# Kernel optimization log

Hardware: AMD Instinct MI355X
Metric: run time of the kernel (lower is better)

Reference implementation:

```python
import jax, jax.numpy as jnp
import numpy as np

EPS = 1e-6
D_CONV = 4

def _layernorm(x):
    m = jnp.mean(x, axis=-1, keepdims=True)
    v = jnp.mean((x - m) ** 2, axis=-1, keepdims=True)
    return (x - m) / jnp.sqrt(v + EPS)

def setup_inputs() -> dict:
    key = jax.random.key(0)
    ks = jax.random.split(key, 20)
    B, L, D = 2, 4096, 1024
    Di = D          # expand = 1
    N = 16          # d_state
    R = 64          # dt_rank = ceil(D/16)
    H = 4 * D       # mlp hidden
    s = 0.02
    rn = lambda k, sh: s * jax.random.normal(k, sh, dtype=jnp.float32)
    x = jax.random.normal(ks[0], (B, L, D), dtype=jnp.float32)
    path = jax.random.permutation(ks[1], L).astype(jnp.int32)
    path_rev = jnp.argsort(path).astype(jnp.int32)
    A_log = jnp.log(jnp.tile(jnp.arange(1, N + 1, dtype=jnp.float32)[None, :], (Di, 1)))
    return {
        'x': x, 'path': path, 'path_rev': path_rev,
        'in_proj_w': rn(ks[2], (2 * Di, D)),
        'conv_w': rn(ks[3], (Di, D_CONV)), 'conv_b': rn(ks[4], (Di,)),
        'x_proj_w': rn(ks[5], (R + 2 * N, Di)),
        'dt_proj_w': rn(ks[6], (Di, R)), 'dt_proj_b': rn(ks[7], (Di,)),
        'A_log': A_log, 'D_param': jnp.ones((Di,), dtype=jnp.float32),
        'out_proj_w': rn(ks[8], (D, Di)),
        'fc1_w': rn(ks[9], (H, D)), 'fc1_b': jnp.zeros((H,), dtype=jnp.float32),
        'fc2_w': rn(ks[10], (D, H)), 'fc2_b': jnp.zeros((D,), dtype=jnp.float32),
    }

def _mamba(u, in_proj_w, conv_w, conv_b, x_proj_w, dt_proj_w, dt_proj_b, A_log, D_param, out_proj_w):
    B, L, _ = u.shape
    N = A_log.shape[1]
    R = dt_proj_w.shape[1]
    xz = u @ in_proj_w.T                      # (B,L,2*Di)
    xi, z = jnp.split(xz, 2, axis=-1)
    # causal depthwise conv1d, kernel 4
    xpad = jnp.pad(xi, ((0, 0), (D_CONV - 1, 0), (0, 0)))
    xc = conv_b + sum(conv_w[:, k] * xpad[:, k:k + L, :] for k in range(D_CONV))
    xc = jax.nn.silu(xc)                      # (B,L,Di)
    proj = xc @ x_proj_w.T                    # (B,L,R+2N)
    dt_r = proj[..., :R]
    Bm = proj[..., R:R + N]                   # (B,L,N)
    Cm = proj[..., R + N:]                    # (B,L,N)
    dt = jax.nn.softplus(dt_r @ dt_proj_w.T + dt_proj_b)  # (B,L,Di)
    A = -jnp.exp(A_log)                       # (Di,N)

    def step(h, inp):
        dt_t, B_t, C_t, x_t = inp             # (B,Di),(B,N),(B,N),(B,Di)
        dA = jnp.exp(dt_t[:, :, None] * A)    # (B,Di,N)
        h = dA * h + (dt_t * x_t)[:, :, None] * B_t[:, None, :]
        y = jnp.einsum('bdn,bn->bd', h, C_t)
        return h, y

    h0 = jnp.zeros((B, xc.shape[-1], N), dtype=u.dtype)
    xs = (dt.transpose(1, 0, 2), Bm.transpose(1, 0, 2), Cm.transpose(1, 0, 2), xc.transpose(1, 0, 2))
    _, ys = jax.lax.scan(step, h0, xs)        # (L,B,Di)
    y = ys.transpose(1, 0, 2) + D_param * xc
    y = y * jax.nn.silu(z)
    return y @ out_proj_w.T

def reference(x, path, path_rev, in_proj_w, conv_w, conv_b, x_proj_w, dt_proj_w, dt_proj_b,
              A_log, D_param, out_proj_w, fc1_w, fc1_b, fc2_w, fc2_b):
    tmp1 = x[:, path, :]                      # zigzag gather
    tmp1 = _mamba(_layernorm(tmp1), in_proj_w, conv_w, conv_b, x_proj_w,
                  dt_proj_w, dt_proj_b, A_log, D_param, out_proj_w)
    x = x + tmp1[:, path_rev, :]              # zigzag scatter (inverse gather)
    h = _layernorm(x)
    h = jax.nn.gelu(h @ fc1_w.T + fc1_b, approximate=True) @ fc2_w.T + fc2_b
    return x + h
```

## Files before the change

### kernel.cpp

```cpp
#include <hip/hip_runtime.h>
#include <cstdint>
#include <cstddef>

typedef unsigned short u16;
typedef __bf16 bf16x8 __attribute__((ext_vector_type(8)));
typedef float f32x4 __attribute__((ext_vector_type(4)));

#define B_ 2
#define L_ 4096
#define D_ 1024
#define N_ 16
#define BL_ 8192
#define NC_ 64
#define LC_ 64

__device__ __forceinline__ float bf2f(u16 h) {
  union { unsigned int u; float f; } v; v.u = ((unsigned int)h) << 16; return v.f;
}
__device__ __forceinline__ u16 f2bf(float f) {
  union { float f; unsigned int u; } v; v.f = f;
  unsigned int r = v.u + 0x7FFFu + ((v.u >> 16) & 1u);
  return (u16)(r >> 16);
}
__device__ __forceinline__ float sigmoidf_(float x) { return 1.0f / (1.0f + __expf(-x)); }

#define WBF_TOT 11730944
__global__ __launch_bounds__(256) void cvt_w_k(
    const float* __restrict__ s0, const float* __restrict__ s1,
    const float* __restrict__ s2, const float* __restrict__ s3,
    const float* __restrict__ s4, const float* __restrict__ s5,
    u16* __restrict__ dst)
{
  int i = blockIdx.x * 256 + threadIdx.x;
  if (i >= WBF_TOT) return;
  float v;
  if (i < 2097152) v = s0[i];
  else if (i < 2228224) { int j = i - 2097152; v = (j < 98304) ? s1[j] : 0.0f; }
  else if (i < 2293760) v = s2[i - 2228224];
  else if (i < 3342336) v = s3[i - 2293760];
  else if (i < 7536640) v = s4[i - 3342336];
  else v = s5[i - 7536640];
  dst[i] = f2bf(v);
}

#define BM 128
#define BN 128
#define BK 32

enum { M_BF16 = 0, M_PROJ = 1, M_SOFTPLUS = 2, M_GELU = 3, M_BIASRES = 4 };

#define GLDS(gp, lp) __builtin_amdgcn_global_load_lds( \
    (const __attribute__((address_space(1))) void*)(gp), \
    (__attribute__((address_space(3))) void*)(lp), 16, 0, 0)

template<int MODE>
__global__ __launch_bounds__(256) void gemm_bt(
    const u16* __restrict__ A, const u16* __restrict__ W,
    float* __restrict__ C, u16* __restrict__ C2,
    const float* __restrict__ bias, const float* __restrict__ resid,
    int M, int N, int K)
{
  __shared__ __align__(16) u16 As[2][BM * BK];
  __shared__ __align__(16) u16 Bs[2][BN * BK];

  const int id = blockIdx.x + gridDim.x * blockIdx.y;
  const int xcd = id & 7;
  const int q = id >> 3;
  const int bandH = gridDim.y >> 3;
  const int xs = q % gridDim.x;
  const int ys = xcd * bandH + q / gridDim.x;
  const int bm = ys * BM;
  const int bn = xs * BN;

  const int tid = threadIdx.x;
  const int lane = tid & 63;
  const int wave = tid >> 6;
  const int wr = (wave >> 1) * 64;
  const int wc = (wave & 1) * 64;

  f32x4 acc[4][4];
#pragma unroll
  for (int i = 0; i < 4; ++i)
#pragma unroll
    for (int j = 0; j < 4; ++j)
#pragma unroll
      for (int r = 0; r < 4; ++r) acc[i][j][r] = 0.0f;

  const int r0 = tid >> 2;
  const int ke = (tid & 3) << 3;
  const u16* Ab = A + (size_t)(bm + r0) * K + ke;
  const u16* Wb = W + (size_t)(bn + r0) * K + ke;
  const size_t rstep = (size_t)64 * K;

  auto issue = [&](int buf, int k0) {
    GLDS(Ab + k0, &As[buf][tid * 8]);
    GLDS(Ab + k0 + rstep, &As[buf][(tid + 256) * 8]);
    GLDS(Wb + k0, &Bs[buf][tid * 8]);
    GLDS(Wb + k0 + rstep, &Bs[buf][(tid + 256) * 8]);
  };

  issue(0, 0);
  int cur = 0;
  const int kq = (lane >> 4) << 3;
  const int mr = lane & 15;
  for (int k0 = 0; k0 < K; k0 += BK) {
    __syncthreads();
    if (k0 + BK < K) issue(cur ^ 1, k0 + BK);
    bf16x8 af[4], bfr[4];
#pragma unroll
    for (int i = 0; i < 4; ++i)
      af[i] = *(const bf16x8*)(&As[cur][(wr + i * 16 + mr) * BK + kq]);
#pragma unroll
    for (int j = 0; j < 4; ++j)
      bfr[j] = *(const bf16x8*)(&Bs[cur][(wc + j * 16 + mr) * BK + kq]);
#pragma unroll
    for (int i = 0; i < 4; ++i)
#pragma unroll
      for (int j = 0; j < 4; ++j)
        acc[i][j] = __builtin_amdgcn_mfma_f32_16x16x32_bf16(af[i], bfr[j], acc[i][j], 0, 0, 0);
    cur ^= 1;
  }

  const int mlo = (lane >> 4) << 2;
  const int nlo = lane & 15;
#pragma unroll
  for (int i = 0; i < 4; ++i) {
#pragma unroll
    for (int j = 0; j < 4; ++j) {
      int col = bn + wc + j * 16 + nlo;
      if (col < N) {
#pragma unroll
        for (int r = 0; r < 4; ++r) {
          int row = bm + wr + i * 16 + mlo + r;
          float v = acc[i][j][r];
          if constexpr (MODE == M_BF16) {
            C2[(size_t)row * N + col] = f2bf(v);
          } else if constexpr (MODE == M_PROJ) {
            C[(size_t)row * 96 + col] = v;
            if (col < 64) C2[((size_t)row << 6) + col] = f2bf(v);
          } else if constexpr (MODE == M_SOFTPLUS) {
            v += bias[col];
            C[(size_t)row * N + col] = (v > 20.0f) ? v : log1pf(__expf(v));
          } else if constexpr (MODE == M_GELU) {
            v += bias[col];
            float a = 0.7978845608028654f * (v + 0.044715f * v * v * v);
            float t = 1.0f - 2.0f / (__expf(2.0f * a) + 1.0f);
            C2[(size_t)row * N + col] = f2bf(0.5f * v * (1.0f + t));
          } else if constexpr (MODE == M_BIASRES) {
            C[(size_t)row * N + col] = v + bias[col] + resid[(size_t)row * N + col];
          }
        }
      }
    }
  }
}

__device__ __forceinline__ void blockReduce2(float& s, float& q) {
#pragma unroll
  for (int o = 32; o > 0; o >>= 1) { s += __shfl_down(s, o, 64); q += __shfl_down(q, o, 64); }
  __shared__ float red[2][4];
  int lane = threadIdx.x & 63, wave = threadIdx.x >> 6;
  if (lane == 0) { red[0][wave] = s; red[1][wave] = q; }
  __syncthreads();
  s = red[0][0] + red[0][1] + red[0][2] + red[0][3];
  q = red[1][0] + red[1][1] + red[1][2] + red[1][3];
}

__global__ __launch_bounds__(256) void ln_gather_k(
    const float* __restrict__ x, const int* __restrict__ path, u16* __restrict__ out)
{
  int b = blockIdx.x >> 12;
  int l = blockIdx.x & 4095;
  int src = path[l];
  const float* row = x + (((size_t)b * L_ + src) << 10);
  u16* orow = out + (((size_t)b * L_ + l) << 10);
  float v[4], s = 0.f, q = 0.f;
#pragma unroll
  for (int i = 0; i < 4; ++i) {
    v[i] = row[threadIdx.x + (i << 8)];
    s += v[i]; q += v[i] * v[i];
  }
  blockReduce2(s, q);
  float mean = s * (1.0f / 1024.0f);
  float var = q * (1.0f / 1024.0f) - mean * mean;
  float rstd = rsqrtf(var + 1e-6f);
#pragma unroll
  for (int i = 0; i < 4; ++i)
    orow[threadIdx.x + (i << 8)] = f2bf((v[i] - mean) * rstd);
}

__global__ __launch_bounds__(256) void ln_scatter_k(
    const float* __restrict__ x, const int* __restrict__ prev,
    const u16* __restrict__ mo, float* __restrict__ xnew, u16* __restrict__ lnout)
{
  int b = blockIdx.x >> 12;
  int l = blockIdx.x & 4095;
  int pl = prev[l];
  const float* xr = x + (((size_t)b * L_ + l) << 10);
  const u16* mr_ = mo + (((size_t)b * L_ + pl) << 10);
  size_t base = ((size_t)blockIdx.x) << 10;
  float v[4], s = 0.f, q = 0.f;
#pragma unroll
  for (int i = 0; i < 4; ++i) {
    v[i] = xr[threadIdx.x + (i << 8)] + bf2f(mr_[threadIdx.x + (i << 8)]);
    s += v[i]; q += v[i] * v[i];
  }
  blockReduce2(s, q);
  float mean = s * (1.0f / 1024.0f);
  float var = q * (1.0f / 1024.0f) - mean * mean;
  float rstd = rsqrtf(var + 1e-6f);
#pragma unroll
  for (int i = 0; i < 4; ++i) {
    xnew[base + threadIdx.x + (i << 8)] = v[i];
    lnout[base + threadIdx.x + (i << 8)] = f2bf((v[i] - mean) * rstd);
  }
}

__global__ __launch_bounds__(256) void conv_silu_k(
    const u16* __restrict__ xz, const float* __restrict__ cw, const float* __restrict__ cb,
    u16* __restrict__ xc)
{
  int idx = blockIdx.x * 256 + threadIdx.x;
  int d = idx & 1023;
  int l = (idx >> 10) & 4095;
  int b = idx >> 22;
  float acc = cb[d];
#pragma unroll
  for (int k = 0; k < 4; ++k) {
    int ls = l + k - 3;
    if (ls >= 0)
      acc += cw[(d << 2) + k] * bf2f(xz[(((size_t)b * L_ + ls) << 11) + d]);
  }
  acc = acc * sigmoidf_(acc);
  xc[idx] = f2bf(acc);
}

__global__ __launch_bounds__(256) void scan_p1_k(
    const float* __restrict__ dt, const u16* __restrict__ xc, const float* __restrict__ proj,
    const float* __restrict__ A_log, float* __restrict__ acum, float* __restrict__ hloc)
{
  int c = blockIdx.x & (NC_ - 1);
  int q = (blockIdx.x >> 6) & 3;
  int b = blockIdx.x >> 8;
  int d = (q << 8) + threadIdx.x;
  float Arow[N_];
#pragma unroll
  for (int n = 0; n < N_; ++n) Arow[n] = -__expf(A_log[(d << 4) + n]);
  float h[N_], ac[N_];
#pragma unroll
  for (int n = 0; n < N_; ++n) { h[n] = 0.0f; ac[n] = 1.0f; }
  int l0 = c << 6;
  for (int i = 0; i < LC_; ++i) {
    size_t rowb = (size_t)b * L_ + (l0 + i);
    float dtv = dt[(rowb << 10) + d];
    float xv = bf2f(xc[(rowb << 10) + d]);
    float dtx = dtv * xv;
    const float* Bp = proj + rowb * 96 + 64;
#pragma unroll
    for (int n = 0; n < N_; ++n) {
      float dA = __expf(dtv * Arow[n]);
      h[n] = dA * h[n] + dtx * Bp[n];
      ac[n] *= dA;
    }
  }
  size_t sb = ((((size_t)b << 10) + d) << 10) + (c << 4);
#pragma unroll
  for (int n = 0; n < N_; ++n) { acum[sb + n] = ac[n]; hloc[sb + n] = h[n]; }
}

__global__ __launch_bounds__(256) void scan_p2_k(
    const float* __restrict__ acum, const float* __restrict__ hloc, float* __restrict__ hin)
{
  int idx = blockIdx.x * 256 + threadIdx.x;
  int n = idx & 15;
  int dn = idx >> 4;
  size_t base = ((size_t)dn << 10) + n;
  float hs = 0.0f;
  for (int c = 0; c < NC_; ++c) {
    hin[base + (c << 4)] = hs;
    hs = acum[base + (c << 4)] * hs + hloc[base + (c << 4)];
  }
}

__global__ __launch_bounds__(256) void scan_p3_k(
    const float* __restrict__ dt, const u16* __restrict__ xc, const float* __restrict__ proj,
    const float* __restrict__ A_log, const float* __restrict__ Dp, const float* __restrict__ hin,
    const u16* __restrict__ xz, u16* __restrict__ yg)
{
  int c = blockIdx.x & (NC_ - 1);
  int q = (blockIdx.x >> 6) & 3;
  int b = blockIdx.x >> 8;
  int d = (q << 8) + threadIdx.x;
  float Arow[N_];
#pragma unroll
  for (int n = 0; n < N_; ++n) Arow[n] = -__expf(A_log[(d << 4) + n]);
  float h[N_];
  size_t sb = ((((size_t)b << 10) + d) << 10) + (c << 4);
#pragma unroll
  for (int n = 0; n < N_; ++n) h[n] = hin[sb + n];
  float Dv = Dp[d];
  int l0 = c << 6;
  for (int i = 0; i < LC_; ++i) {
    size_t rowb = (size_t)b * L_ + (l0 + i);
    float dtv = dt[(rowb << 10) + d];
    float xv = bf2f(xc[(rowb << 10) + d]);
    float dtx = dtv * xv;
    const float* Bp = proj + rowb * 96 + 64;
    const float* Cp = proj + rowb * 96 + 80;
    float y = 0.0f;
#pragma unroll
    for (int n = 0; n < N_; ++n) {
      float dA = __expf(dtv * Arow[n]);
      h[n] = dA * h[n] + dtx * Bp[n];
      y += h[n] * Cp[n];
    }
    y += Dv * xv;
    float zv = bf2f(xz[(rowb << 11) + 1024 + d]);
    yg[(rowb << 10) + d] = f2bf(y * zv * sigmoidf_(zv));
  }
}

extern "C" void kernel_launch(void* const* d_in, const int* in_sizes, int n_in,
                              void* d_out, int out_size, void* d_ws, size_t ws_size,
                              hipStream_t stream)
{
  const float* x_in      = (const float*)d_in[0];
  const int*   path      = (const int*)d_in[1];
  const int*   path_rev  = (const int*)d_in[2];
  const float* in_proj_w = (const float*)d_in[3];
  const float* conv_w    = (const float*)d_in[4];
  const float* conv_b    = (const float*)d_in[5];
  const float* x_proj_w  = (const float*)d_in[6];
  const float* dt_proj_w = (const float*)d_in[7];
  const float* dt_proj_b = (const float*)d_in[8];
  const float* A_log     = (const float*)d_in[9];
  const float* Dp        = (const float*)d_in[10];
  const float* out_pw    = (const float*)d_in[11];
  const float* fc1_w     = (const float*)d_in[12];
  const float* fc1_b     = (const float*)d_in[13];
  const float* fc2_w     = (const float*)d_in[14];
  const float* fc2_b     = (const float*)d_in[15];
  float* out = (float*)d_out;

  char* w = (char*)d_ws;
  size_t off = 0;
  auto alloc = [&](size_t bytes) -> char* {
    char* p = w + off;
    off = (off + bytes + 255) & ~(size_t)255;
    return p;
  };
  u16*   wbf   = (u16*)  alloc((size_t)WBF_TOT * 2);
  u16*   ln_bf = (u16*)  alloc((size_t)BL_ * 1024 * 2);
  u16*   xz    = (u16*)  alloc((size_t)BL_ * 2048 * 2);
  u16*   xc    = (u16*)  alloc((size_t)BL_ * 1024 * 2);
  char*  pool0 = alloc(0);
  float* proj  = (float*)alloc((size_t)BL_ * 96 * 4);
  u16*   dtr   = (u16*)  alloc((size_t)BL_ * 64 * 2);
  float* dt    = (float*)alloc((size_t)BL_ * 1024 * 4);
  float* acum  = (float*)alloc((size_t)2 * 1024 * NC_ * 16 * 4);
  float* hloc  = (float*)alloc((size_t)2 * 1024 * NC_ * 16 * 4);
  float* hin   = (float*)alloc((size_t)2 * 1024 * NC_ * 16 * 4);
  u16*   yg    = (u16*)  alloc((size_t)BL_ * 1024 * 2);
  float* xnew  = (float*)alloc((size_t)BL_ * 1024 * 4);
  u16*   mo    = xz;
  u16*   h1b   = (u16*)pool0;

  const u16* w_inp = wbf;
  const u16* w_xp  = wbf + 2097152;
  const u16* w_dtp = wbf + 2228224;
  const u16* w_op  = wbf + 2293760;
  const u16* w_fc1 = wbf + 3342336;
  const u16* w_fc2 = wbf + 7536640;

  dim3 blk(256);
  cvt_w_k<<<WBF_TOT / 256, blk, 0, stream>>>(in_proj_w, x_proj_w, dt_proj_w, out_pw,
                                             fc1_w, fc2_w, wbf);
  ln_gather_k<<<BL_, blk, 0, stream>>>(x_in, path, ln_bf);
  gemm_bt<M_BF16><<<dim3(16, 64), blk, 0, stream>>>(ln_bf, w_inp, nullptr, xz, nullptr, nullptr, 8192, 2048, 1024);
  conv_silu_k<<<(BL_ * 1024) / 256, blk, 0, stream>>>(xz, conv_w, conv_b, xc);
  gemm_bt<M_PROJ><<<dim3(1, 64), blk, 0, stream>>>(xc, w_xp, proj, dtr, nullptr, nullptr, 8192, 96, 1024);
  gemm_bt<M_SOFTPLUS><<<dim3(8, 64), blk, 0, stream>>>(dtr, w_dtp, dt, nullptr, dt_proj_b, nullptr, 8192, 1024, 64);
  scan_p1_k<<<2 * 4 * NC_, blk, 0, stream>>>(dt, xc, proj, A_log, acum, hloc);
  scan_p2_k<<<(2 * 1024 * 16) / 256, blk, 0, stream>>>(acum, hloc, hin);
  scan_p3_k<<<2 * 4 * NC_, blk, 0, stream>>>(dt, xc, proj, A_log, Dp, hin, xz, yg);
  gemm_bt<M_BF16><<<dim3(8, 64), blk, 0, stream>>>(yg, w_op, nullptr, mo, nullptr, nullptr, 8192, 1024, 1024);
  ln_scatter_k<<<BL_, blk, 0, stream>>>(x_in, path_rev, mo, xnew, ln_bf);
  gemm_bt<M_GELU><<<dim3(32, 64), blk, 0, stream>>>(ln_bf, w_fc1, nullptr, h1b, fc1_b, nullptr, 8192, 4096, 1024);
  gemm_bt<M_BIASRES><<<dim3(8, 64), blk, 0, stream>>>(h1b, w_fc2, out, nullptr, fc2_b, xnew, 8192, 1024, 4096);
}
```

Measured before the change: 638.2 us.

## Triple-buffer GEMM LDS pipeline and store dt and residual in bf16

The GEMM K-loop moves from double to triple buffering. Loads are issued two stages ahead, and __syncthreads is replaced with an explicit vmcnt wait plus s_barrier, so global-to-LDS loads overlap more with MFMA work. Separately, the softplus dt output and the xnew residual are stored as bf16 instead of fp32, which halves their memory traffic in the scan kernels and the fc2 epilogue. The trade-off is lower precision in dt and the residual, more LDS per block (possibly lower occupancy), and a workspace layout where xnew now sits after the h1b region.

```diff
diff --git a/kernel.cpp b/kernel.cpp
--- a/kernel.cpp
+++ b/kernel.cpp
@@ -57,11 +57,11 @@
 __global__ __launch_bounds__(256) void gemm_bt(
     const u16* __restrict__ A, const u16* __restrict__ W,
     float* __restrict__ C, u16* __restrict__ C2,
-    const float* __restrict__ bias, const float* __restrict__ resid,
+    const float* __restrict__ bias, const u16* __restrict__ resid,
     int M, int N, int K)
 {
-  __shared__ __align__(16) u16 As[2][BM * BK];
-  __shared__ __align__(16) u16 Bs[2][BN * BK];
+  __shared__ __align__(16) u16 As[3][BM * BK];
+  __shared__ __align__(16) u16 Bs[3][BN * BK];
 
   const int id = blockIdx.x + gridDim.x * blockIdx.y;
   const int xcd = id & 7;
@@ -100,12 +100,16 @@
   };
 
   issue(0, 0);
+  if (BK < K) issue(1, BK);
   int cur = 0;
   const int kq = (lane >> 4) << 3;
   const int mr = lane & 15;
   for (int k0 = 0; k0 < K; k0 += BK) {
-    __syncthreads();
-    if (k0 + BK < K) issue(cur ^ 1, k0 + BK);
+    if (k0 + BK < K) asm volatile("s_waitcnt vmcnt(4)" ::: "memory");
+    else             asm volatile("s_waitcnt vmcnt(0)" ::: "memory");
+    asm volatile("s_barrier" ::: "memory");
+    int nb = cur + 2; if (nb >= 3) nb -= 3;
+    if (k0 + 2 * BK < K) issue(nb, k0 + 2 * BK);
     bf16x8 af[4], bfr[4];
 #pragma unroll
     for (int i = 0; i < 4; ++i)
@@ -118,7 +122,7 @@
 #pragma unroll
       for (int j = 0; j < 4; ++j)
         acc[i][j] = __builtin_amdgcn_mfma_f32_16x16x32_bf16(af[i], bfr[j], acc[i][j], 0, 0, 0);
-    cur ^= 1;
+    ++cur; if (cur == 3) cur = 0;
   }
 
   const int mlo = (lane >> 4) << 2;
@@ -140,14 +144,15 @@
             if (col < 64) C2[((size_t)row << 6) + col] = f2bf(v);
           } else if constexpr (MODE == M_SOFTPLUS) {
             v += bias[col];
-            C[(size_t)row * N + col] = (v > 20.0f) ? v : log1pf(__expf(v));
+            v = (v > 20.0f) ? v : log1pf(__expf(v));
+            C2[(size_t)row * N + col] = f2bf(v);
           } else if constexpr (MODE == M_GELU) {
             v += bias[col];
             float a = 0.7978845608028654f * (v + 0.044715f * v * v * v);
             float t = 1.0f - 2.0f / (__expf(2.0f * a) + 1.0f);
             C2[(size_t)row * N + col] = f2bf(0.5f * v * (1.0f + t));
           } else if constexpr (MODE == M_BIASRES) {
-            C[(size_t)row * N + col] = v + bias[col] + resid[(size_t)row * N + col];
+            C[(size_t)row * N + col] = v + bias[col] + bf2f(resid[(size_t)row * N + col]);
           }
         }
       }
@@ -191,7 +196,7 @@
 
 __global__ __launch_bounds__(256) void ln_scatter_k(
     const float* __restrict__ x, const int* __restrict__ prev,
-    const u16* __restrict__ mo, float* __restrict__ xnew, u16* __restrict__ lnout)
+    const u16* __restrict__ mo, u16* __restrict__ xnew, u16* __restrict__ lnout)
 {
   int b = blockIdx.x >> 12;
   int l = blockIdx.x & 4095;
@@ -211,7 +216,7 @@
   float rstd = rsqrtf(var + 1e-6f);
 #pragma unroll
   for (int i = 0; i < 4; ++i) {
-    xnew[base + threadIdx.x + (i << 8)] = v[i];
+    xnew[base + threadIdx.x + (i << 8)] = f2bf(v[i]);
     lnout[base + threadIdx.x + (i << 8)] = f2bf((v[i] - mean) * rstd);
   }
 }
@@ -236,7 +241,7 @@
 }
 
 __global__ __launch_bounds__(256) void scan_p1_k(
-    const float* __restrict__ dt, const u16* __restrict__ xc, const float* __restrict__ proj,
+    const u16* __restrict__ dt, const u16* __restrict__ xc, const float* __restrict__ proj,
     const float* __restrict__ A_log, float* __restrict__ acum, float* __restrict__ hloc)
 {
   int c = blockIdx.x & (NC_ - 1);
@@ -252,7 +257,7 @@
   int l0 = c << 6;
   for (int i = 0; i < LC_; ++i) {
     size_t rowb = (size_t)b * L_ + (l0 + i);
-    float dtv = dt[(rowb << 10) + d];
+    float dtv = bf2f(dt[(rowb << 10) + d]);
     float xv = bf2f(xc[(rowb << 10) + d]);
     float dtx = dtv * xv;
     const float* Bp = proj + rowb * 96 + 64;
@@ -283,7 +288,7 @@
 }
 
 __global__ __launch_bounds__(256) void scan_p3_k(
-    const float* __restrict__ dt, const u16* __restrict__ xc, const float* __restrict__ proj,
+    const u16* __restrict__ dt, const u16* __restrict__ xc, const float* __restrict__ proj,
     const float* __restrict__ A_log, const float* __restrict__ Dp, const float* __restrict__ hin,
     const u16* __restrict__ xz, u16* __restrict__ yg)
 {
@@ -302,7 +307,7 @@
   int l0 = c << 6;
   for (int i = 0; i < LC_; ++i) {
     size_t rowb = (size_t)b * L_ + (l0 + i);
-    float dtv = dt[(rowb << 10) + d];
+    float dtv = bf2f(dt[(rowb << 10) + d]);
     float xv = bf2f(xc[(rowb << 10) + d]);
     float dtx = dtv * xv;
     const float* Bp = proj + rowb * 96 + 64;
@@ -356,14 +361,15 @@
   char*  pool0 = alloc(0);
   float* proj  = (float*)alloc((size_t)BL_ * 96 * 4);
   u16*   dtr   = (u16*)  alloc((size_t)BL_ * 64 * 2);
-  float* dt    = (float*)alloc((size_t)BL_ * 1024 * 4);
+  u16*   dt    = (u16*)  alloc((size_t)BL_ * 1024 * 2);
   float* acum  = (float*)alloc((size_t)2 * 1024 * NC_ * 16 * 4);
   float* hloc  = (float*)alloc((size_t)2 * 1024 * NC_ * 16 * 4);
   float* hin   = (float*)alloc((size_t)2 * 1024 * NC_ * 16 * 4);
   u16*   yg    = (u16*)  alloc((size_t)BL_ * 1024 * 2);
-  float* xnew  = (float*)alloc((size_t)BL_ * 1024 * 4);
+  u16*   h1b   = (u16*)pool0;
+  off = (size_t)(pool0 - w) + ((size_t)BL_ * 4096 * 2);
+  u16*   xnew  = (u16*)  alloc((size_t)BL_ * 1024 * 2);
   u16*   mo    = xz;
-  u16*   h1b   = (u16*)pool0;
 
   const u16* w_inp = wbf;
   const u16* w_xp  = wbf + 2097152;
@@ -379,7 +385,7 @@
   gemm_bt<M_BF16><<<dim3(16, 64), blk, 0, stream>>>(ln_bf, w_inp, nullptr, xz, nullptr, nullptr, 8192, 2048, 1024);
   conv_silu_k<<<(BL_ * 1024) / 256, blk, 0, stream>>>(xz, conv_w, conv_b, xc);
   gemm_bt<M_PROJ><<<dim3(1, 64), blk, 0, stream>>>(xc, w_xp, proj, dtr, nullptr, nullptr, 8192, 96, 1024);
-  gemm_bt<M_SOFTPLUS><<<dim3(8, 64), blk, 0, stream>>>(dtr, w_dtp, dt, nullptr, dt_proj_b, nullptr, 8192, 1024, 64);
+  gemm_bt<M_SOFTPLUS><<<dim3(8, 64), blk, 0, stream>>>(dtr, w_dtp, nullptr, dt, dt_proj_b, nullptr, 8192, 1024, 64);
   scan_p1_k<<<2 * 4 * NC_, blk, 0, stream>>>(dt, xc, proj, A_log, acum, hloc);
   scan_p2_k<<<(2 * 1024 * 16) / 256, blk, 0, stream>>>(acum, hloc, hin);
   scan_p3_k<<<2 * 4 * NC_, blk, 0, stream>>>(dt, xc, proj, A_log, Dp, hin, xz, yg);
```

Result: no change. 633.0 us (-0.8%).
